# Kernel optimization log

Hardware: AMD Instinct MI355X
Metric: run time of the kernel (lower is better)

## Reference

```python
import jax, jax.numpy as jnp
import numpy as np

BN_EPS = 1e-3  # O-CNN default bn_eps


def setup_inputs() -> dict:
    key = jax.random.key(0)
    k1, k2, k3 = jax.random.split(key, 3)
    N, Cin, Cout, K = 100000, 32, 32, 27  # nodes, channels, 3x3x3 taps
    data_in = jax.random.normal(k1, (1, Cin, N, 1), dtype=jnp.float32)
    neigh = jax.random.randint(k2, (N, K), 0, N, dtype=jnp.int32)
    weight = jax.random.normal(k3, (K, Cin, Cout), dtype=jnp.float32) * 0.05
    gamma = jnp.ones((Cout,), dtype=jnp.float32)
    beta = jnp.zeros((Cout,), dtype=jnp.float32)
    return {"data_in": data_in, "neigh": neigh, "weight": weight,
            "gamma": gamma, "beta": beta}


def reference(data_in, neigh, weight, gamma, beta):
    # data_in: [1, Cin, N, 1] -> x: [N, Cin]
    x = data_in[0, :, :, 0].T
    # Octree conv: gather 27 neighbor features per node, then small matmul.
    col = x[neigh]                                   # [N, 27, Cin] (irregular gather)
    y = jnp.einsum('nkc,kcd->nd', col, weight)       # [N, Cout]
    # BatchNorm2d in training mode: stats over the N (spatial) axis.
    mean = jnp.mean(y, axis=0)
    var = jnp.mean(jnp.square(y - mean), axis=0)     # biased variance, as BN uses
    yn = (y - mean) * jax.lax.rsqrt(var + BN_EPS) * gamma + beta
    # back to O-CNN layout [1, Cout, N, 1]
    return yn.T[None, :, :, None]
```

## Files before the change

### kernel.cpp

```cpp
#include <hip/hip_runtime.h>

#define KK 27

typedef short bf16x8 __attribute__((ext_vector_type(8)));
typedef float f32x4  __attribute__((ext_vector_type(4)));

__device__ inline unsigned short f2bf(float f) {
    unsigned u = __float_as_uint(f);
    unsigned r = u + 0x7fffu + ((u >> 16) & 1u);
    return (unsigned short)(r >> 16);
}

__global__ __launch_bounds__(256) void xprep_k(const float* __restrict__ in,
                                               unsigned short* __restrict__ xTb, int N) {
    __shared__ float tile[32][33];
    int n0 = blockIdx.x * 32;
    int tx = threadIdx.x & 31;
    int ty = threadIdx.x >> 5;
#pragma unroll
    for (int c = ty; c < 32; c += 8) {
        int n = n0 + tx;
        tile[c][tx] = (n < N) ? in[(long)c * N + n] : 0.f;
    }
    __syncthreads();
#pragma unroll
    for (int nn = ty; nn < 32; nn += 8) {
        int n = n0 + nn;
        if (n < N) xTb[(long)n * 32 + tx] = f2bf(tile[tx][nn]);
    }
}

__global__ __launch_bounds__(256) void wprep_k(const float* __restrict__ w,
                                               unsigned short* __restrict__ wTb) {
    int k = blockIdx.x;
    for (int i = threadIdx.x; i < 1024; i += 256) {
        int cin = i >> 5, cout = i & 31;
        wTb[k * 1024 + cout * 32 + cin] = f2bf(w[k * 1024 + cin * 32 + cout]);
    }
}

__global__ __launch_bounds__(64, 4) void conv_k(const unsigned short* __restrict__ xTb,
                                                const int* __restrict__ neigh,
                                                const unsigned short* __restrict__ wTb,
                                                float* __restrict__ y,
                                                float* __restrict__ partial,
                                                int N, int nrows) {
    __shared__ float ct[32][33];

    const int L    = threadIdx.x;
    const int r16  = L & 15;
    const int quad = L >> 4;
    const int base = blockIdx.x * 32;
    const int n0 = base + r16;
    const int n1 = base + 16 + r16;
    const bool v0 = (n0 < N), v1 = (n1 < N);
    const long nb0 = (long)(v0 ? n0 : 0) * KK;
    const long nb1 = (long)(v1 ? n1 : 0) * KK;

    const bf16x8 zz = {0, 0, 0, 0, 0, 0, 0, 0};

    f32x4 acc00 = {0.f, 0.f, 0.f, 0.f};
    f32x4 acc01 = acc00, acc10 = acc00, acc11 = acc00;

    int ia = neigh[nb0];
    int ib = neigh[nb1];
    int ja = neigh[nb0 + 1];
    int jb = neigh[nb1 + 1];

    bf16x8 a0 = *(const bf16x8*)(xTb + (long)ia * 32 + quad * 8);
    bf16x8 a1 = *(const bf16x8*)(xTb + (long)ib * 32 + quad * 8);
    bf16x8 b0 = *(const bf16x8*)(wTb + r16 * 32 + quad * 8);
    bf16x8 b1 = *(const bf16x8*)(wTb + (16 + r16) * 32 + quad * 8);
    a0 = v0 ? a0 : zz;
    a1 = v1 ? a1 : zz;

#pragma unroll 1
    for (int k = 0; k < KK; ++k) {
        bf16x8 na0 = zz, na1 = zz, pb0 = zz, pb1 = zz;
        if (k < KK - 1) {
            na0 = *(const bf16x8*)(xTb + (long)ja * 32 + quad * 8);
            na1 = *(const bf16x8*)(xTb + (long)jb * 32 + quad * 8);
            const unsigned short* wn = wTb + (k + 1) * 1024;
            pb0 = *(const bf16x8*)(wn + r16 * 32 + quad * 8);
            pb1 = *(const bf16x8*)(wn + (16 + r16) * 32 + quad * 8);
            int kk = (k + 2 < KK) ? (k + 2) : (KK - 1);
            ja = neigh[nb0 + kk];
            jb = neigh[nb1 + kk];
        }

        acc00 = __builtin_amdgcn_mfma_f32_16x16x32_bf16(a0, b0, acc00, 0, 0, 0);
        acc01 = __builtin_amdgcn_mfma_f32_16x16x32_bf16(a0, b1, acc01, 0, 0, 0);
        acc10 = __builtin_amdgcn_mfma_f32_16x16x32_bf16(a1, b0, acc10, 0, 0, 0);
        acc11 = __builtin_amdgcn_mfma_f32_16x16x32_bf16(a1, b1, acc11, 0, 0, 0);

        if (k < KK - 1) {
            a0 = v0 ? na0 : zz;
            a1 = v1 ? na1 : zz;
            b0 = pb0;
            b1 = pb1;
        }
    }

    float s0 = 0.f, q0 = 0.f, s1 = 0.f, q1 = 0.f;
#pragma unroll
    for (int r = 0; r < 4; ++r) {
        s0 += acc00[r] + acc10[r];
        q0 += acc00[r] * acc00[r] + acc10[r] * acc10[r];
        s1 += acc01[r] + acc11[r];
        q1 += acc01[r] * acc01[r] + acc11[r] * acc11[r];
    }
#pragma unroll
    for (int off = 16; off < 64; off <<= 1) {
        s0 += __shfl_xor(s0, off, 64);
        q0 += __shfl_xor(q0, off, 64);
        s1 += __shfl_xor(s1, off, 64);
        q1 += __shfl_xor(q1, off, 64);
    }
    if (L < 16) {
        const int b = blockIdx.x;
        partial[(long)L * nrows + b]        = s0;
        partial[(long)(L + 16) * nrows + b] = s1;
        partial[(long)(L + 32) * nrows + b] = q0;
        partial[(long)(L + 48) * nrows + b] = q1;
    }

#pragma unroll
    for (int r = 0; r < 4; ++r) {
        ct[quad * 4 + r][r16]           = acc00[r];
        ct[quad * 4 + r][16 + r16]      = acc01[r];
        ct[16 + quad * 4 + r][r16]      = acc10[r];
        ct[16 + quad * 4 + r][16 + r16] = acc11[r];
    }
    __syncthreads();
    const int node = L & 31;
    const int half = L >> 5;
    const int gn = base + node;
#pragma unroll
    for (int i = 0; i < 16; ++i) {
        const int cout = i * 2 + half;
        if (gn < N) y[(long)cout * N + gn] = ct[node][cout];
    }
}

__global__ __launch_bounds__(256) void stats1_k(const float* __restrict__ partial,
                                                int nrows, float* __restrict__ tot) {
    __shared__ float red[256];
    const int col = blockIdx.x;
    const float* row = partial + (long)col * nrows;
    float s = 0.f;
    for (int r = threadIdx.x; r < nrows; r += 256) s += row[r];
    red[threadIdx.x] = s;
    __syncthreads();
    for (int w = 128; w >= 64; w >>= 1) {
        if (threadIdx.x < w) red[threadIdx.x] += red[threadIdx.x + w];
        __syncthreads();
    }
    if (threadIdx.x < 64) {
        float v = red[threadIdx.x];
#pragma unroll
        for (int off = 1; off < 64; off <<= 1) v += __shfl_xor(v, off, 64);
        if (threadIdx.x == 0) tot[col] = v;
    }
}

__global__ __launch_bounds__(256) void norm_k(float* __restrict__ y,
                                              const float* __restrict__ tot,
                                              const float* __restrict__ gamma,
                                              const float* __restrict__ beta, int N) {
    const int d = blockIdx.y;
    const float mean = tot[d] / (float)N;
    const float var  = tot[d + 32] / (float)N - mean * mean;
    const float sc   = gamma[d] * rsqrtf(var + 1e-3f);
    const float sh   = beta[d] - mean * sc;

    int i = blockIdx.x * blockDim.x + threadIdx.x;
    int base = i * 4;
    if (base + 3 < N) {
        float4* p = (float4*)(y + (long)d * N + base);
        float4 v = *p;
        v.x = fmaf(v.x, sc, sh);
        v.y = fmaf(v.y, sc, sh);
        v.z = fmaf(v.z, sc, sh);
        v.w = fmaf(v.w, sc, sh);
        *p = v;
    } else if (base < N) {
        for (int t = base; t < N; ++t) y[(long)d * N + t] = fmaf(y[(long)d * N + t], sc, sh);
    }
}

extern "C" void kernel_launch(void* const* d_in, const int* in_sizes, int n_in,
                              void* d_out, int out_size, void* d_ws, size_t ws_size,
                              hipStream_t stream) {
    const float* data_in = (const float*)d_in[0];
    const int*   neigh   = (const int*)d_in[1];
    const float* weight  = (const float*)d_in[2];
    const float* gamma   = (const float*)d_in[3];
    const float* beta    = (const float*)d_in[4];
    float* out = (float*)d_out;

    const int N = in_sizes[1] / KK;
    const int nblk  = (N + 31) / 32;
    const int nrows = nblk;

    char* ws = (char*)d_ws;
    unsigned short* xTb = (unsigned short*)ws;
    unsigned short* wTb = (unsigned short*)(ws + (size_t)N * 64);
    float* partial = (float*)(ws + (size_t)N * 64 + 55296);
    float* tot     = partial + (size_t)64 * nrows;

    xprep_k<<<nblk, 256, 0, stream>>>(data_in, xTb, N);
    wprep_k<<<KK, 256, 0, stream>>>(weight, wTb);
    conv_k<<<nblk, 64, 0, stream>>>(xTb, neigh, wTb, out, partial, N, nrows);
    stats1_k<<<64, 256, 0, stream>>>(partial, nrows, tot);
    dim3 ngrid(((N + 3) / 4 + 255) / 256, 32);
    norm_k<<<ngrid, 256, 0, stream>>>(out, tot, gamma, beta, N);
}
```

Before: 136.9 us.

## Merge prep kernels and restructure conv to 16 nodes per wave

Fuses the x-transpose and weight-prep kernels into one launch, with block-index dispatch, to remove one kernel launch. The conv kernel now runs 4 independent waves of 16 nodes each per 256-thread block instead of one 32-node wave per block. This doubles the number of waves so more gathers are in flight. It also replaces the block barrier with a per-wave LDS wait and doubles the partial-stats rows. The trade-off is fewer MFMAs per gathered weight load, with B operands reloaded per wave, and a longer stats reduction.

```diff
diff --git a/kernel.cpp b/kernel.cpp
--- a/kernel.cpp
+++ b/kernel.cpp
@@ -11,10 +11,21 @@
     return (unsigned short)(r >> 16);
 }
 
-__global__ __launch_bounds__(256) void xprep_k(const float* __restrict__ in,
-                                               unsigned short* __restrict__ xTb, int N) {
+__global__ __launch_bounds__(256) void prep_k(const float* __restrict__ in,
+                                              const float* __restrict__ w,
+                                              unsigned short* __restrict__ xTb,
+                                              unsigned short* __restrict__ wTb,
+                                              int N) {
+    const int bx = blockIdx.x;
+    if (bx < KK) {
+        for (int i = threadIdx.x; i < 1024; i += 256) {
+            int cin = i >> 5, cout = i & 31;
+            wTb[bx * 1024 + cout * 32 + cin] = f2bf(w[bx * 1024 + cin * 32 + cout]);
+        }
+        return;
+    }
     __shared__ float tile[32][33];
-    int n0 = blockIdx.x * 32;
+    int n0 = (bx - KK) * 32;
     int tx = threadIdx.x & 31;
     int ty = threadIdx.x >> 5;
 #pragma unroll
@@ -30,115 +41,87 @@
     }
 }
 
-__global__ __launch_bounds__(256) void wprep_k(const float* __restrict__ w,
-                                               unsigned short* __restrict__ wTb) {
-    int k = blockIdx.x;
-    for (int i = threadIdx.x; i < 1024; i += 256) {
-        int cin = i >> 5, cout = i & 31;
-        wTb[k * 1024 + cout * 32 + cin] = f2bf(w[k * 1024 + cin * 32 + cout]);
-    }
-}
-
-__global__ __launch_bounds__(64, 4) void conv_k(const unsigned short* __restrict__ xTb,
-                                                const int* __restrict__ neigh,
-                                                const unsigned short* __restrict__ wTb,
-                                                float* __restrict__ y,
-                                                float* __restrict__ partial,
-                                                int N, int nrows) {
-    __shared__ float ct[32][33];
-
-    const int L    = threadIdx.x;
-    const int r16  = L & 15;
-    const int quad = L >> 4;
-    const int base = blockIdx.x * 32;
-    const int n0 = base + r16;
-    const int n1 = base + 16 + r16;
-    const bool v0 = (n0 < N), v1 = (n1 < N);
-    const long nb0 = (long)(v0 ? n0 : 0) * KK;
-    const long nb1 = (long)(v1 ? n1 : 0) * KK;
-
-    const bf16x8 zz = {0, 0, 0, 0, 0, 0, 0, 0};
-
-    f32x4 acc00 = {0.f, 0.f, 0.f, 0.f};
-    f32x4 acc01 = acc00, acc10 = acc00, acc11 = acc00;
-
-    int ia = neigh[nb0];
-    int ib = neigh[nb1];
-    int ja = neigh[nb0 + 1];
-    int jb = neigh[nb1 + 1];
-
-    bf16x8 a0 = *(const bf16x8*)(xTb + (long)ia * 32 + quad * 8);
-    bf16x8 a1 = *(const bf16x8*)(xTb + (long)ib * 32 + quad * 8);
+__global__ __launch_bounds__(256) void conv_k(const unsigned short* __restrict__ xTb,
+                                              const int* __restrict__ neigh,
+                                              const unsigned short* __restrict__ wTb,
+                                              float* __restrict__ y,
+                                              float* __restrict__ partial,
+                                              int N, int nrows) {
+    __shared__ float ct[4][16][33];
+
+    const int tid   = threadIdx.x;
+    const int L     = tid & 63;
+    const int wv    = tid >> 6;
+    const int r16   = L & 15;
+    const int quad  = L >> 4;
+    const int base2 = blockIdx.x * 64 + wv * 16;
+    const int nc    = min(base2 + r16, N - 1);
+    const long nb   = (long)nc * KK;
+
+    f32x4 acc0 = {0.f, 0.f, 0.f, 0.f};
+    f32x4 acc1 = acc0;
+
+    int m = neigh[nb];
+    bf16x8 a  = *(const bf16x8*)(xTb + (long)m * 32 + quad * 8);
     bf16x8 b0 = *(const bf16x8*)(wTb + r16 * 32 + quad * 8);
     bf16x8 b1 = *(const bf16x8*)(wTb + (16 + r16) * 32 + quad * 8);
-    a0 = v0 ? a0 : zz;
-    a1 = v1 ? a1 : zz;
+    int j = neigh[nb + 1];
 
 #pragma unroll 1
     for (int k = 0; k < KK; ++k) {
-        bf16x8 na0 = zz, na1 = zz, pb0 = zz, pb1 = zz;
-        if (k < KK - 1) {
-            na0 = *(const bf16x8*)(xTb + (long)ja * 32 + quad * 8);
-            na1 = *(const bf16x8*)(xTb + (long)jb * 32 + quad * 8);
+        bf16x8 na, pb0, pb1;
+        if (k + 1 < KK) {
+            na = *(const bf16x8*)(xTb + (long)j * 32 + quad * 8);
             const unsigned short* wn = wTb + (k + 1) * 1024;
             pb0 = *(const bf16x8*)(wn + r16 * 32 + quad * 8);
             pb1 = *(const bf16x8*)(wn + (16 + r16) * 32 + quad * 8);
-            int kk = (k + 2 < KK) ? (k + 2) : (KK - 1);
-            ja = neigh[nb0 + kk];
-            jb = neigh[nb1 + kk];
+            j = neigh[nb + min(k + 2, KK - 1)];
         }
 
-        acc00 = __builtin_amdgcn_mfma_f32_16x16x32_bf16(a0, b0, acc00, 0, 0, 0);
-        acc01 = __builtin_amdgcn_mfma_f32_16x16x32_bf16(a0, b1, acc01, 0, 0, 0);
-        acc10 = __builtin_amdgcn_mfma_f32_16x16x32_bf16(a1, b0, acc10, 0, 0, 0);
-        acc11 = __builtin_amdgcn_mfma_f32_16x16x32_bf16(a1, b1, acc11, 0, 0, 0);
-
-        if (k < KK - 1) {
-            a0 = v0 ? na0 : zz;
-            a1 = v1 ? na1 : zz;
-            b0 = pb0;
-            b1 = pb1;
+        acc0 = __builtin_amdgcn_mfma_f32_16x16x32_bf16(a, b0, acc0, 0, 0, 0);
+        acc1 = __builtin_amdgcn_mfma_f32_16x16x32_bf16(a, b1, acc1, 0, 0, 0);
+
+        if (k + 1 < KK) { a = na; b0 = pb0; b1 = pb1; }
+    }
+
+#pragma unroll
+    for (int r = 0; r < 4; ++r) {
+        if (base2 + quad * 4 + r >= N) { acc0[r] = 0.f; acc1[r] = 0.f; }
+    }
+
+    float s0 = 0.f, q0 = 0.f, s1 = 0.f, q1 = 0.f;
+#pragma unroll
+    for (int r = 0; r < 4; ++r) {
+        s0 += acc0[r];  q0 += acc0[r] * acc0[r];
+        s1 += acc1[r];  q1 += acc1[r] * acc1[r];
+    }
+    s0 += __shfl_xor(s0, 16, 64); q0 += __shfl_xor(q0, 16, 64);
+    s1 += __shfl_xor(s1, 16, 64); q1 += __shfl_xor(q1, 16, 64);
+    s0 += __shfl_xor(s0, 32, 64); q0 += __shfl_xor(q0, 32, 64);
+    s1 += __shfl_xor(s1, 32, 64); q1 += __shfl_xor(q1, 32, 64);
+    const int wrow = blockIdx.x * 4 + wv;
+    if (L < 16) {
+        partial[(long)L * nrows + wrow]        = s0;
+        partial[(long)(L + 16) * nrows + wrow] = s1;
+        partial[(long)(L + 32) * nrows + wrow] = q0;
+        partial[(long)(L + 48) * nrows + wrow] = q1;
+    }
+
+#pragma unroll
+    for (int r = 0; r < 4; ++r) {
+        ct[wv][quad * 4 + r][r16]      = acc0[r];
+        ct[wv][quad * 4 + r][16 + r16] = acc1[r];
+    }
+    asm volatile("s_waitcnt lgkmcnt(0)" ::: "memory");
+    const int node  = L & 15;
+    const int cbase = (L >> 4) * 8;
+    const int gn = base2 + node;
+    if (gn < N) {
+#pragma unroll
+        for (int c = 0; c < 8; ++c) {
+            const int cout = cbase + c;
+            y[(long)cout * N + gn] = ct[wv][node][cout];
         }
-    }
-
-    float s0 = 0.f, q0 = 0.f, s1 = 0.f, q1 = 0.f;
-#pragma unroll
-    for (int r = 0; r < 4; ++r) {
-        s0 += acc00[r] + acc10[r];
-        q0 += acc00[r] * acc00[r] + acc10[r] * acc10[r];
-        s1 += acc01[r] + acc11[r];
-        q1 += acc01[r] * acc01[r] + acc11[r] * acc11[r];
-    }
-#pragma unroll
-    for (int off = 16; off < 64; off <<= 1) {
-        s0 += __shfl_xor(s0, off, 64);
-        q0 += __shfl_xor(q0, off, 64);
-        s1 += __shfl_xor(s1, off, 64);
-        q1 += __shfl_xor(q1, off, 64);
-    }
-    if (L < 16) {
-        const int b = blockIdx.x;
-        partial[(long)L * nrows + b]        = s0;
-        partial[(long)(L + 16) * nrows + b] = s1;
-        partial[(long)(L + 32) * nrows + b] = q0;
-        partial[(long)(L + 48) * nrows + b] = q1;
-    }
-
-#pragma unroll
-    for (int r = 0; r < 4; ++r) {
-        ct[quad * 4 + r][r16]           = acc00[r];
-        ct[quad * 4 + r][16 + r16]      = acc01[r];
-        ct[16 + quad * 4 + r][r16]      = acc10[r];
-        ct[16 + quad * 4 + r][16 + r16] = acc11[r];
-    }
-    __syncthreads();
-    const int node = L & 31;
-    const int half = L >> 5;
-    const int gn = base + node;
-#pragma unroll
-    for (int i = 0; i < 16; ++i) {
-        const int cout = i * 2 + half;
-        if (gn < N) y[(long)cout * N + gn] = ct[node][cout];
     }
 }
 
@@ -199,8 +182,9 @@
     float* out = (float*)d_out;
 
     const int N = in_sizes[1] / KK;
-    const int nblk  = (N + 31) / 32;
-    const int nrows = nblk;
+    const int nblk32 = (N + 31) / 32;
+    const int nblk64 = (N + 63) / 64;
+    const int nrows  = nblk64 * 4;
 
     char* ws = (char*)d_ws;
     unsigned short* xTb = (unsigned short*)ws;
@@ -208,9 +192,8 @@
     float* partial = (float*)(ws + (size_t)N * 64 + 55296);
     float* tot     = partial + (size_t)64 * nrows;
 
-    xprep_k<<<nblk, 256, 0, stream>>>(data_in, xTb, N);
-    wprep_k<<<KK, 256, 0, stream>>>(weight, wTb);
-    conv_k<<<nblk, 64, 0, stream>>>(xTb, neigh, wTb, out, partial, N, nrows);
+    prep_k<<<KK + nblk32, 256, 0, stream>>>(data_in, weight, xTb, wTb, N);
+    conv_k<<<nblk64, 256, 0, stream>>>(xTb, neigh, wTb, out, partial, N, nrows);
     stats1_k<<<64, 256, 0, stream>>>(partial, nrows, tot);
     dim3 ngrid(((N + 3) / 4 + 255) / 256, 32);
     norm_k<<<ngrid, 256, 0, stream>>>(out, tot, gamma, beta, N);
```

Measured after the change: 146.0 us. +6.6%, slower.
